# Kernel optimization log

Measured on AMD Instinct MI355X. Metric: run time of the kernel, lower is better.

The kernel has to match this reference:

```python
import jax, jax.numpy as jnp
import numpy as np

NUM_BINS = 20
TEMPERATURE = 0.1
EPS = 1e-8


def setup_inputs() -> dict:
    key = jax.random.key(0)
    k1, k2 = jax.random.split(key)
    shape = (32, 1, 1024, 1024)  # B, C, H, W segmentation-style probability maps
    preds = jax.random.uniform(k1, shape, dtype=jnp.float32)
    targets = jax.random.uniform(k2, shape, dtype=jnp.float32)
    return {"preds": preds, "targets": targets}


def reference(preds, targets):
    p = preds.reshape(-1)
    t = targets.reshape(-1)
    centers = jnp.linspace(0.0, 1.0, NUM_BINS, dtype=p.dtype)

    def per_bin(c):
        # Gaussian soft-assignment weights for this bin center
        w = jnp.exp(-(p - c) ** 2 / TEMPERATURE)
        w_sum = w.sum()
        e = (w * p).sum() / (w_sum + EPS)  # weighted mean confidence
        o = (w * t).sum() / (w_sum + EPS)  # weighted mean accuracy
        # torch code skips bins with zero total weight
        return jnp.where(w_sum == 0.0, jnp.zeros_like(e), jnp.abs(e - o))

    # lax.map loops sequentially over the 20 bin centers so we never
    # materialize a [NUM_BINS, N] weight matrix.
    contribs = jax.lax.map(per_bin, centers)
    return contribs.sum() / NUM_BINS
```

## Files before the change

### kernel.cpp

```cpp
#include <hip/hip_runtime.h>
#include <math.h>

#define NUM_BINS 20
#define NACC     (3 * NUM_BINS)
#define BLOCK    256
#define NBLK     1024

__device__ __host__ constexpr float K1f() { return (float)(-1.0 / (0.1 * 0.6931471805599453)); }
__device__ __host__ constexpr float K2f() { return (float)( 2.0 / (1.9 * 0.6931471805599453)); }

__global__ __launch_bounds__(BLOCK) void ace_partial(const float* __restrict__ p,
                                                     const float* __restrict__ t,
                                                     float* __restrict__ partials,
                                                     int n4) {
    const float K1 = K1f();
    const float K2 = K2f();

    float aW[NUM_BINS], aP[NUM_BINS], aT[NUM_BINS];
#pragma unroll
    for (int j = 0; j < NUM_BINS; ++j) { aW[j] = 0.f; aP[j] = 0.f; aT[j] = 0.f; }

    const float4* __restrict__ p4 = (const float4*)p;
    const float4* __restrict__ t4 = (const float4*)t;

    int tid    = blockIdx.x * BLOCK + threadIdx.x;
    int stride = gridDim.x * BLOCK;

    for (int i = tid; i < n4; i += stride) {
        float4 pv = p4[i];
        float4 tv = t4[i];

        float pe[4] = {pv.x, pv.y, pv.z, pv.w};
        float te[4] = {tv.x, tv.y, tv.z, tv.w};

#pragma unroll
        for (int e = 0; e < 4; ++e) {
            float pp = pe[e];
            float tt = te[e];
            float u  = __builtin_amdgcn_exp2f(K1 * pp * pp);
            float G  = __builtin_amdgcn_exp2f(K2 * pp);
            float g  = u;
#pragma unroll
            for (int j = 0; j < NUM_BINS; ++j) {
                aW[j] += g;
                aP[j]  = fmaf(g, pp, aP[j]);
                aT[j]  = fmaf(g, tt, aT[j]);
                g     *= G;
            }
        }
    }

#pragma unroll
    for (int j = 0; j < NUM_BINS; ++j) {
#pragma unroll
        for (int off = 32; off > 0; off >>= 1) {
            aW[j] += __shfl_down(aW[j], off, 64);
            aP[j] += __shfl_down(aP[j], off, 64);
            aT[j] += __shfl_down(aT[j], off, 64);
        }
    }

    __shared__ float red[BLOCK / 64][NACC];
    int wave = threadIdx.x >> 6;
    int lane = threadIdx.x & 63;
    if (lane == 0) {
#pragma unroll
        for (int j = 0; j < NUM_BINS; ++j) {
            red[wave][j]                = aW[j];
            red[wave][NUM_BINS + j]     = aP[j];
            red[wave][2 * NUM_BINS + j] = aT[j];
        }
    }
    __syncthreads();

    if (threadIdx.x < NACC) {
        float s = 0.f;
#pragma unroll
        for (int w = 0; w < BLOCK / 64; ++w) s += red[w][threadIdx.x];
        partials[blockIdx.x * NACC + threadIdx.x] = s;
    }
}

__global__ __launch_bounds__(1024) void ace_final(const float* __restrict__ partials,
                                                  float* __restrict__ out) {
    const float K1 = K1f();

    __shared__ float red[NACC][16];
    __shared__ float sums[NACC];
    int tid = threadIdx.x;

    if (tid < NACC * 16) {
        int j = tid >> 4;
        int k = tid & 15;
        float s = 0.f;
        for (int b = k; b < NBLK; b += 16) s += partials[b * NACC + j];
        red[j][k] = s;
    }
    __syncthreads();

    if (tid < NACC) {
        float s = 0.f;
#pragma unroll
        for (int k = 0; k < 16; ++k) s += red[tid][k];
        sums[tid] = s;
    }
    __syncthreads();

    if (tid == 0) {
        float acc = 0.f;
        for (int j = 0; j < NUM_BINS; ++j) {
            float c    = (float)j / 19.0f;
            float A    = __builtin_amdgcn_exp2f(K1 * c * c);
            float wsum = A * sums[j];
            float denom = wsum + 1e-8f;
            float e    = (A * sums[NUM_BINS + j]) / denom;
            float o    = (A * sums[2 * NUM_BINS + j]) / denom;
            float contrib = (wsum == 0.0f) ? 0.0f : fabsf(e - o);
            acc += contrib;
        }
        out[0] = acc / (float)NUM_BINS;
    }
}

extern "C" void kernel_launch(void* const* d_in, const int* in_sizes, int n_in,
                              void* d_out, int out_size, void* d_ws, size_t ws_size,
                              hipStream_t stream) {
    const float* preds   = (const float*)d_in[0];
    const float* targets = (const float*)d_in[1];
    float* out           = (float*)d_out;
    float* partials      = (float*)d_ws;

    int n  = in_sizes[0];
    int n4 = n >> 2;

    ace_partial<<<NBLK, BLOCK, 0, stream>>>(preds, targets, partials, n4);
    ace_final<<<1, 1024, 0, stream>>>(partials, out);
}
```

Measured before the change: 301.2 us.

## Replace per-element Gaussian bin weights with fine histogram plus Taylor correction

Instead of evaluating 20 Gaussian weights per element, each element is scattered into a 1024-bin shared-memory histogram of count, sum p and sum t, using LDS atomics. The histograms are reduced across blocks, and a final kernel rebuilds the 20 soft-bin sums from bin midpoints with a first-order Taylor correction. This aims to remove the per-element exp and 60-FMA inner loop, making the kernel closer to memory-bound. In exchange it adds atomic contention, a third launch, a grid size taken from the workspace size, and approximation error. Inputs outside [0,1] are clamped into edge bins.

```diff
diff --git a/kernel.cpp b/kernel.cpp
--- a/kernel.cpp
+++ b/kernel.cpp
@@ -2,51 +2,107 @@
 #include <math.h>
 
 #define NUM_BINS 20
-#define NACC     (3 * NUM_BINS)
+#define NB       1024
+#define NH       (3 * NB)
 #define BLOCK    256
-#define NBLK     1024
+#define MAXBLK   1024
 
-__device__ __host__ constexpr float K1f() { return (float)(-1.0 / (0.1 * 0.6931471805599453)); }
-__device__ __host__ constexpr float K2f() { return (float)( 2.0 / (1.9 * 0.6931471805599453)); }
+#define K1C (-14.426950408889634f)
 
-__global__ __launch_bounds__(BLOCK) void ace_partial(const float* __restrict__ p,
-                                                     const float* __restrict__ t,
-                                                     float* __restrict__ partials,
-                                                     int n4) {
-    const float K1 = K1f();
-    const float K2 = K2f();
+__device__ __forceinline__ void acc_elem(float pp, float tt,
+                                         float* hN, float* hP, float* hT) {
+    unsigned b = (unsigned)(pp * (float)NB);
+    if (b > NB - 1) b = NB - 1;
+    atomicAdd(&hN[b], 1.0f);
+    atomicAdd(&hP[b], pp);
+    atomicAdd(&hT[b], tt);
+}
 
-    float aW[NUM_BINS], aP[NUM_BINS], aT[NUM_BINS];
-#pragma unroll
-    for (int j = 0; j < NUM_BINS; ++j) { aW[j] = 0.f; aP[j] = 0.f; aT[j] = 0.f; }
+__global__ __launch_bounds__(BLOCK) void ace_hist(const float* __restrict__ p,
+                                                  const float* __restrict__ t,
+                                                  float* __restrict__ partials,
+                                                  int n4, int nblk) {
+    __shared__ float hN[NB];
+    __shared__ float hP[NB];
+    __shared__ float hT[NB];
+    for (int i = threadIdx.x; i < NB; i += BLOCK) { hN[i] = 0.f; hP[i] = 0.f; hT[i] = 0.f; }
+    __syncthreads();
 
     const float4* __restrict__ p4 = (const float4*)p;
     const float4* __restrict__ t4 = (const float4*)t;
 
     int tid    = blockIdx.x * BLOCK + threadIdx.x;
-    int stride = gridDim.x * BLOCK;
+    int stride = nblk * BLOCK;
 
-    for (int i = tid; i < n4; i += stride) {
-        float4 pv = p4[i];
-        float4 tv = t4[i];
+    int i0 = tid;
+    for (; i0 + stride < n4; i0 += 2 * stride) {
+        float4 a0 = p4[i0];
+        float4 b0 = t4[i0];
+        float4 a1 = p4[i0 + stride];
+        float4 b1 = t4[i0 + stride];
+        acc_elem(a0.x, b0.x, hN, hP, hT);
+        acc_elem(a0.y, b0.y, hN, hP, hT);
+        acc_elem(a0.z, b0.z, hN, hP, hT);
+        acc_elem(a0.w, b0.w, hN, hP, hT);
+        acc_elem(a1.x, b1.x, hN, hP, hT);
+        acc_elem(a1.y, b1.y, hN, hP, hT);
+        acc_elem(a1.z, b1.z, hN, hP, hT);
+        acc_elem(a1.w, b1.w, hN, hP, hT);
+    }
+    for (; i0 < n4; i0 += stride) {
+        float4 a0 = p4[i0];
+        float4 b0 = t4[i0];
+        acc_elem(a0.x, b0.x, hN, hP, hT);
+        acc_elem(a0.y, b0.y, hN, hP, hT);
+        acc_elem(a0.z, b0.z, hN, hP, hT);
+        acc_elem(a0.w, b0.w, hN, hP, hT);
+    }
 
-        float pe[4] = {pv.x, pv.y, pv.z, pv.w};
-        float te[4] = {tv.x, tv.y, tv.z, tv.w};
+    __syncthreads();
 
+    float* dst = partials + (size_t)blockIdx.x * NH;
+    for (int i = threadIdx.x; i < NB; i += BLOCK) {
+        dst[i]          = hN[i];
+        dst[NB + i]     = hP[i];
+        dst[2 * NB + i] = hT[i];
+    }
+}
+
+__global__ __launch_bounds__(BLOCK) void ace_reduce(const float* __restrict__ partials,
+                                                    float* __restrict__ hist,
+                                                    int nblk) {
+    int col = blockIdx.x * BLOCK + threadIdx.x;
+    if (col >= NH) return;
+    float s = 0.f;
+    for (int b = 0; b < nblk; ++b) s += partials[(size_t)b * NH + col];
+    hist[col] = s;
+}
+
+__global__ __launch_bounds__(BLOCK) void ace_final(const float* __restrict__ hist,
+                                                   float* __restrict__ out) {
+    const float* HN = hist;
+    const float* HP = hist + NB;
+    const float* HT = hist + 2 * NB;
+
+    float Sw[NUM_BINS], Sp[NUM_BINS], St[NUM_BINS];
 #pragma unroll
-        for (int e = 0; e < 4; ++e) {
-            float pp = pe[e];
-            float tt = te[e];
-            float u  = __builtin_amdgcn_exp2f(K1 * pp * pp);
-            float G  = __builtin_amdgcn_exp2f(K2 * pp);
-            float g  = u;
+    for (int j = 0; j < NUM_BINS; ++j) { Sw[j] = 0.f; Sp[j] = 0.f; St[j] = 0.f; }
+
+    for (int b = threadIdx.x; b < NB; b += BLOCK) {
+        float n  = HN[b];
+        float P  = HP[b];
+        float T  = HT[b];
+        float m  = ((float)b + 0.5f) * (1.0f / (float)NB);
+        float dp = P - m * n;
 #pragma unroll
-            for (int j = 0; j < NUM_BINS; ++j) {
-                aW[j] += g;
-                aP[j]  = fmaf(g, pp, aP[j]);
-                aT[j]  = fmaf(g, tt, aT[j]);
-                g     *= G;
-            }
+        for (int j = 0; j < NUM_BINS; ++j) {
+            float c  = (float)j * (1.0f / 19.0f);
+            float d  = m - c;
+            float w  = __builtin_amdgcn_exp2f(K1C * d * d);
+            float wd = w * (-20.0f * d);
+            Sw[j] += w * n + wd * dp;
+            Sp[j] += w * P + wd * m * dp;
+            St[j] += w * T;
         }
     }
 
@@ -54,69 +110,39 @@
     for (int j = 0; j < NUM_BINS; ++j) {
 #pragma unroll
         for (int off = 32; off > 0; off >>= 1) {
-            aW[j] += __shfl_down(aW[j], off, 64);
-            aP[j] += __shfl_down(aP[j], off, 64);
-            aT[j] += __shfl_down(aT[j], off, 64);
+            Sw[j] += __shfl_down(Sw[j], off, 64);
+            Sp[j] += __shfl_down(Sp[j], off, 64);
+            St[j] += __shfl_down(St[j], off, 64);
         }
     }
 
-    __shared__ float red[BLOCK / 64][NACC];
+    __shared__ float red[BLOCK / 64][3 * NUM_BINS];
     int wave = threadIdx.x >> 6;
     int lane = threadIdx.x & 63;
     if (lane == 0) {
 #pragma unroll
         for (int j = 0; j < NUM_BINS; ++j) {
-            red[wave][j]                = aW[j];
-            red[wave][NUM_BINS + j]     = aP[j];
-            red[wave][2 * NUM_BINS + j] = aT[j];
+            red[wave][j]                = Sw[j];
+            red[wave][NUM_BINS + j]     = Sp[j];
+            red[wave][2 * NUM_BINS + j] = St[j];
         }
     }
     __syncthreads();
 
-    if (threadIdx.x < NACC) {
-        float s = 0.f;
-#pragma unroll
-        for (int w = 0; w < BLOCK / 64; ++w) s += red[w][threadIdx.x];
-        partials[blockIdx.x * NACC + threadIdx.x] = s;
-    }
-}
-
-__global__ __launch_bounds__(1024) void ace_final(const float* __restrict__ partials,
-                                                  float* __restrict__ out) {
-    const float K1 = K1f();
-
-    __shared__ float red[NACC][16];
-    __shared__ float sums[NACC];
-    int tid = threadIdx.x;
-
-    if (tid < NACC * 16) {
-        int j = tid >> 4;
-        int k = tid & 15;
-        float s = 0.f;
-        for (int b = k; b < NBLK; b += 16) s += partials[b * NACC + j];
-        red[j][k] = s;
-    }
-    __syncthreads();
-
-    if (tid < NACC) {
-        float s = 0.f;
-#pragma unroll
-        for (int k = 0; k < 16; ++k) s += red[tid][k];
-        sums[tid] = s;
-    }
-    __syncthreads();
-
-    if (tid == 0) {
+    if (threadIdx.x == 0) {
         float acc = 0.f;
         for (int j = 0; j < NUM_BINS; ++j) {
-            float c    = (float)j / 19.0f;
-            float A    = __builtin_amdgcn_exp2f(K1 * c * c);
-            float wsum = A * sums[j];
-            float denom = wsum + 1e-8f;
-            float e    = (A * sums[NUM_BINS + j]) / denom;
-            float o    = (A * sums[2 * NUM_BINS + j]) / denom;
-            float contrib = (wsum == 0.0f) ? 0.0f : fabsf(e - o);
-            acc += contrib;
+            float sw = 0.f, sp = 0.f, st = 0.f;
+#pragma unroll
+            for (int w = 0; w < BLOCK / 64; ++w) {
+                sw += red[w][j];
+                sp += red[w][NUM_BINS + j];
+                st += red[w][2 * NUM_BINS + j];
+            }
+            float denom = sw + 1e-8f;
+            float e = sp / denom;
+            float o = st / denom;
+            acc += (sw == 0.0f) ? 0.0f : fabsf(e - o);
         }
         out[0] = acc / (float)NUM_BINS;
     }
@@ -128,11 +154,19 @@
     const float* preds   = (const float*)d_in[0];
     const float* targets = (const float*)d_in[1];
     float* out           = (float*)d_out;
-    float* partials      = (float*)d_ws;
 
     int n  = in_sizes[0];
     int n4 = n >> 2;
 
-    ace_partial<<<NBLK, BLOCK, 0, stream>>>(preds, targets, partials, n4);
-    ace_final<<<1, 1024, 0, stream>>>(partials, out);
+    size_t histBytes = (size_t)NH * sizeof(float);
+    long nblk = (long)(ws_size / histBytes) - 1;
+    if (nblk > MAXBLK) nblk = MAXBLK;
+    if (nblk < 1) nblk = 1;
+
+    float* partials = (float*)d_ws;
+    float* hist     = partials + (size_t)nblk * NH;
+
+    ace_hist<<<(int)nblk, BLOCK, 0, stream>>>(preds, targets, partials, n4, (int)nblk);
+    ace_reduce<<<(NH + BLOCK - 1) / BLOCK, BLOCK, 0, stream>>>(partials, hist, (int)nblk);
+    ace_final<<<1, BLOCK, 0, stream>>>(hist, out);
 }
```

After: 923.6 us. 207% more time.
